# Kernel tuning notes

Hardware: AMD Instinct MI355X
Metric: run time of the kernel (lower is better)

Reference implementation:

```python
import jax, jax.numpy as jnp
import numpy as np

B, T, D, H = 32, 8192, 128, 128

def setup_inputs() -> dict:
    key = jax.random.key(0)
    k1, k2, k3, k4, k5 = jax.random.split(key, 5)
    return {
        "encoder_outputs": jax.random.normal(k1, (B, T, D), dtype=jnp.float32),
        "decoder_hidden": jax.random.normal(k2, (B, H), dtype=jnp.float32),
        "W1": jax.random.normal(k3, (D, D), dtype=jnp.float32) * 0.08,
        "W2": jax.random.normal(k4, (H, D), dtype=jnp.float32) * 0.08,
        "V": jax.random.normal(k5, (D, 1), dtype=jnp.float32) * 0.08,
    }

def reference(encoder_outputs, decoder_hidden, W1, W2, V):
    # score: [B, T, D] = tanh(enc @ W1 + (dec @ W2)[:, None, :])
    score = jnp.tanh(jnp.einsum('btd,de->bte', encoder_outputs, W1)
                     + jnp.einsum('bh,hd->bd', decoder_hidden, W2)[:, None, :])
    # logits: [B, T, 1]; softmax over time axis (axis=1)
    logits = jnp.einsum('btd,do->bto', score, V)
    attention_weights = jax.nn.softmax(logits, axis=1)
    # context: [B, D] weighted sum over T
    context_vector = jnp.sum(attention_weights * encoder_outputs, axis=1)
    return context_vector, attention_weights
```

## Files before the change

kernel.cpp:

```cpp
#include <hip/hip_runtime.h>

#define B_ 32
#define T_ 8192
#define D_ 128
#define MBLK 64
#define NCHUNK 128

typedef __attribute__((ext_vector_type(8))) _Float16 half8;
typedef __attribute__((ext_vector_type(4))) _Float16 half4;
typedef __attribute__((ext_vector_type(4))) float floatx4;

__device__ __forceinline__ float tanh_fast(float x) {
    float e = __expf(2.0f * x);
    return 1.0f - __fdividef(2.0f, e + 1.0f);
}

__global__ void frag_kernel(const float* __restrict__ W1, half8* __restrict__ W1frag) {
    int tg = blockIdx.x * 256 + threadIdx.x;
    int kk = tg >> 9, ni = (tg >> 6) & 7, lane = tg & 63;
    half8 h;
    #pragma unroll
    for (int j = 0; j < 8; ++j) {
        int k = kk * 32 + ((lane >> 4) * 8) + j;
        int n = ni * 16 + (lane & 15);
        h[j] = (_Float16)W1[k * 128 + n];
    }
    W1frag[tg] = h;
}

__global__ void bias_kernel(const float* __restrict__ dec, const float* __restrict__ W2,
                            float* __restrict__ bias) {
    int b = blockIdx.x, d = threadIdx.x;
    float acc = 0.f;
    for (int h = 0; h < 128; ++h)
        acc += dec[b * 128 + h] * W2[h * 128 + d];
    bias[b * 128 + d] = acc;
}

__global__ __launch_bounds__(256)
void main_kernel(const float* __restrict__ enc, const half8* __restrict__ W1frag,
                 const float* __restrict__ bias, const float* __restrict__ V,
                 float* __restrict__ out_w, float* __restrict__ m_part,
                 float* __restrict__ s_part, float* __restrict__ c_part)
{
    __shared__ __align__(16) _Float16 encl[MBLK * 128];
    __shared__ __align__(16) half8 bfr[2048];
    __shared__ float red[MBLK];
    __shared__ float c_red[8 * 128];

    const int tid = threadIdx.x;
    const int l = tid & 63;
    const int w = tid >> 6;
    const int bid = blockIdx.x;
    const int b = bid >> 7;
    const int chunk = bid & 127;
    const float* encp = enc + ((long)(b * T_) + chunk * MBLK) * D_;

    #pragma unroll
    for (int q = 0; q < 8; ++q)
        bfr[q * 256 + tid] = W1frag[q * 256 + tid];

    #pragma unroll
    for (int q = 0; q < 8; ++q) {
        int flat = (q * 256 + tid) * 4;
        int r = flat >> 7, c = flat & 127;
        float4 f = *(const float4*)(encp + flat);
        half4 h;
        h[0] = (_Float16)f.x; h[1] = (_Float16)f.y;
        h[2] = (_Float16)f.z; h[3] = (_Float16)f.w;
        int byte = r * 256 + ((c * 2) ^ ((r & 7) << 4));
        *(half4*)((char*)encl + byte) = h;
    }
    __syncthreads();

    floatx4 acc[8];
    #pragma unroll
    for (int ni = 0; ni < 8; ++ni) acc[ni] = (floatx4)0.0f;

    const int arow = w * 16 + (l & 15);
    const int asw = (arow & 7) << 4;
    const int abase = arow * 256;
    #pragma unroll
    for (int kk = 0; kk < 4; ++kk) {
        half8 a = *(const half8*)((char*)encl +
                   (abase + (((kk * 64) + ((l >> 4) * 16)) ^ asw)));
        #pragma unroll
        for (int ni = 0; ni < 8; ++ni)
            acc[ni] = __builtin_amdgcn_mfma_f32_16x16x32_f16(
                          a, bfr[(kk * 8 + ni) * 64 + l], acc[ni], 0, 0, 0);
    }

    float bs[8], vv[8];
    #pragma unroll
    for (int ni = 0; ni < 8; ++ni) {
        int n = ni * 16 + (l & 15);
        bs[ni] = bias[b * 128 + n];
        vv[ni] = V[n];
    }
    #pragma unroll
    for (int j2 = 0; j2 < 4; ++j2) {
        float p = 0.f;
        #pragma unroll
        for (int ni = 0; ni < 8; ++ni)
            p += tanh_fast(acc[ni][j2] + bs[ni]) * vv[ni];
        #pragma unroll
        for (int mk = 1; mk < 16; mk <<= 1)
            p += __shfl_xor(p, mk);
        if ((l & 15) == 0) {
            int r = w * 16 + (l >> 4) * 4 + j2;
            red[r] = p;
            out_w[(long)b * T_ + chunk * MBLK + r] = p;
        }
    }
    __syncthreads();

    if (tid < 64) {
        float lg = red[tid];
        float m = lg;
        #pragma unroll
        for (int mk = 1; mk < 64; mk <<= 1) m = fmaxf(m, __shfl_xor(m, mk));
        float ew = __expf(lg - m);
        float s = ew;
        #pragma unroll
        for (int mk = 1; mk < 64; mk <<= 1) s += __shfl_xor(s, mk);
        red[tid] = ew;
        if (tid == 0) { m_part[bid] = m; s_part[bid] = s; }
    }
    __syncthreads();

    {
        int c0 = (tid & 31) * 4, rg = tid >> 5;
        floatx4 cc = (floatx4)0.0f;
        #pragma unroll
        for (int rr = 0; rr < 8; ++rr) {
            int r = rg * 8 + rr;
            float wgt = red[r];
            half4 h = *(const half4*)((char*)encl +
                       (r * 256 + (((tid & 31) * 8) ^ ((r & 7) << 4))));
            #pragma unroll
            for (int i = 0; i < 4; ++i) cc[i] += wgt * (float)h[i];
        }
        *(floatx4*)(&c_red[rg * 128 + c0]) = cc;
    }
    __syncthreads();
    if (tid < 128) {
        float s = 0.f;
        #pragma unroll
        for (int g = 0; g < 8; ++g) s += c_red[g * 128 + tid];
        c_part[(long)bid * 128 + tid] = s;
    }
}

__global__ void reduce_kernel(const float* __restrict__ m_part, const float* __restrict__ s_part,
                              const float* __restrict__ c_part, float* __restrict__ ctx,
                              float* __restrict__ mg, float* __restrict__ sg)
{
    __shared__ float sm[128];
    __shared__ float sc[128];
    int b = blockIdx.x, i = threadIdx.x;
    float m = m_part[b * 128 + i];
    sm[i] = m;
    __syncthreads();
    for (int s = 64; s > 0; s >>= 1) {
        if (i < s) sm[i] = fmaxf(sm[i], sm[i + s]);
        __syncthreads();
    }
    float m_g = sm[0];
    __syncthreads();
    float e = __expf(m - m_g);
    sm[i] = s_part[b * 128 + i] * e;
    __syncthreads();
    for (int s = 64; s > 0; s >>= 1) {
        if (i < s) sm[i] += sm[i + s];
        __syncthreads();
    }
    float s_g = sm[0];
    __syncthreads();
    sc[i] = e / s_g;
    if (i == 0) { mg[b] = m_g; sg[b] = s_g; }
    __syncthreads();
    float acc = 0.f;
    for (int ch = 0; ch < 128; ++ch)
        acc += c_part[((long)b * 128 + ch) * 128 + i] * sc[ch];
    ctx[b * 128 + i] = acc;
}

__global__ void finalize_kernel(float* __restrict__ out_w, const float* __restrict__ mg,
                                const float* __restrict__ sg)
{
    int idx = blockIdx.x * 256 + threadIdx.x;
    int b = idx >> 13;
    float lg = out_w[idx];
    out_w[idx] = __expf(lg - mg[b]) / sg[b];
}

extern "C" void kernel_launch(void* const* d_in, const int* in_sizes, int n_in,
                              void* d_out, int out_size, void* d_ws, size_t ws_size,
                              hipStream_t stream)
{
    const float* enc = (const float*)d_in[0];
    const float* dec = (const float*)d_in[1];
    const float* W1  = (const float*)d_in[2];
    const float* W2  = (const float*)d_in[3];
    const float* V   = (const float*)d_in[4];

    float* ctx  = (float*)d_out;
    float* outw = ctx + B_ * D_;

    float* ws     = (float*)d_ws;
    float* bias   = ws;
    float* m_part = bias + 4096;
    float* s_part = m_part + 4096;
    float* mg     = s_part + 4096;
    float* sg     = mg + 32;
    float* c_part = sg + 32;
    half8* W1frag = (half8*)(c_part + (long)B_ * NCHUNK * 128);

    frag_kernel<<<8, 256, 0, stream>>>(W1, W1frag);
    bias_kernel<<<32, 128, 0, stream>>>(dec, W2, bias);
    main_kernel<<<B_ * NCHUNK, 256, 0, stream>>>(enc, W1frag, bias, V, outw, m_part, s_part, c_part);
    reduce_kernel<<<B_, 128, 0, stream>>>(m_part, s_part, c_part, ctx, mg, sg);
    finalize_kernel<<<(B_ * T_) / 256, 256, 0, stream>>>(outw, mg, sg);
}
```

Baseline: 59.12 us.

## Double rows per block, merge prep kernels, halve partial reductions

Each main-kernel block now processes 128 timesteps instead of 64, with each wave computing two 16-row MFMA tiles that share the same B-fragment loads. This halves the grid and the per-block W1 fragment staging overhead, and it halves the partial softmax/context outputs that the reduce kernel must combine. The frag and bias kernels are merged into one prep launch to save a launch. In exchange, LDS per block grows (the fp16 encoder tile doubles) and accumulator register pressure doubles, which may reduce occupancy.

```diff
diff --git a/kernel.cpp b/kernel.cpp
--- a/kernel.cpp
+++ b/kernel.cpp
@@ -3,8 +3,8 @@
 #define B_ 32
 #define T_ 8192
 #define D_ 128
-#define MBLK 64
-#define NCHUNK 128
+#define MBLK 128
+#define NCHUNK 64
 
 typedef __attribute__((ext_vector_type(8))) _Float16 half8;
 typedef __attribute__((ext_vector_type(4))) _Float16 half4;
@@ -15,26 +15,29 @@
     return 1.0f - __fdividef(2.0f, e + 1.0f);
 }
 
-__global__ void frag_kernel(const float* __restrict__ W1, half8* __restrict__ W1frag) {
-    int tg = blockIdx.x * 256 + threadIdx.x;
-    int kk = tg >> 9, ni = (tg >> 6) & 7, lane = tg & 63;
-    half8 h;
-    #pragma unroll
-    for (int j = 0; j < 8; ++j) {
-        int k = kk * 32 + ((lane >> 4) * 8) + j;
-        int n = ni * 16 + (lane & 15);
-        h[j] = (_Float16)W1[k * 128 + n];
-    }
-    W1frag[tg] = h;
-}
-
-__global__ void bias_kernel(const float* __restrict__ dec, const float* __restrict__ W2,
+__global__ void prep_kernel(const float* __restrict__ W1, half8* __restrict__ W1frag,
+                            const float* __restrict__ dec, const float* __restrict__ W2,
                             float* __restrict__ bias) {
-    int b = blockIdx.x, d = threadIdx.x;
-    float acc = 0.f;
-    for (int h = 0; h < 128; ++h)
-        acc += dec[b * 128 + h] * W2[h * 128 + d];
-    bias[b * 128 + d] = acc;
+    int bid = blockIdx.x, tid = threadIdx.x;
+    if (bid < 8) {
+        int tg = bid * 256 + tid;
+        int kk = tg >> 9, ni = (tg >> 6) & 7, lane = tg & 63;
+        half8 h;
+        #pragma unroll
+        for (int j = 0; j < 8; ++j) {
+            int k = kk * 32 + ((lane >> 4) * 8) + j;
+            int n = ni * 16 + (lane & 15);
+            h[j] = (_Float16)W1[k * 128 + n];
+        }
+        W1frag[tg] = h;
+    } else {
+        int b = (bid - 8) * 2 + (tid >> 7);
+        int d = tid & 127;
+        float acc = 0.f;
+        for (int h = 0; h < 128; ++h)
+            acc += dec[b * 128 + h] * W2[h * 128 + d];
+        bias[b * 128 + d] = acc;
+    }
 }
 
 __global__ __launch_bounds__(256)
@@ -52,8 +55,8 @@
     const int l = tid & 63;
     const int w = tid >> 6;
     const int bid = blockIdx.x;
-    const int b = bid >> 7;
-    const int chunk = bid & 127;
+    const int b = bid >> 6;
+    const int chunk = bid & 63;
     const float* encp = enc + ((long)(b * T_) + chunk * MBLK) * D_;
 
     #pragma unroll
@@ -61,7 +64,7 @@
         bfr[q * 256 + tid] = W1frag[q * 256 + tid];
 
     #pragma unroll
-    for (int q = 0; q < 8; ++q) {
+    for (int q = 0; q < 16; ++q) {
         int flat = (q * 256 + tid) * 4;
         int r = flat >> 7, c = flat & 127;
         float4 f = *(const float4*)(encp + flat);
@@ -73,21 +76,25 @@
     }
     __syncthreads();
 
-    floatx4 acc[8];
-    #pragma unroll
-    for (int ni = 0; ni < 8; ++ni) acc[ni] = (floatx4)0.0f;
-
-    const int arow = w * 16 + (l & 15);
+    floatx4 acc[2][8];
+    #pragma unroll
+    for (int si = 0; si < 2; ++si)
+        #pragma unroll
+        for (int ni = 0; ni < 8; ++ni) acc[si][ni] = (floatx4)0.0f;
+
+    const int arow = w * 32 + (l & 15);
     const int asw = (arow & 7) << 4;
-    const int abase = arow * 256;
     #pragma unroll
     for (int kk = 0; kk < 4; ++kk) {
-        half8 a = *(const half8*)((char*)encl +
-                   (abase + (((kk * 64) + ((l >> 4) * 16)) ^ asw)));
-        #pragma unroll
-        for (int ni = 0; ni < 8; ++ni)
-            acc[ni] = __builtin_amdgcn_mfma_f32_16x16x32_f16(
-                          a, bfr[(kk * 8 + ni) * 64 + l], acc[ni], 0, 0, 0);
+        int koff = (kk * 64 + ((l >> 4) * 16)) ^ asw;
+        half8 a0 = *(const half8*)((char*)encl + (arow * 256 + koff));
+        half8 a1 = *(const half8*)((char*)encl + ((arow + 16) * 256 + koff));
+        #pragma unroll
+        for (int ni = 0; ni < 8; ++ni) {
+            half8 bf = bfr[(kk * 8 + ni) * 64 + l];
+            acc[0][ni] = __builtin_amdgcn_mfma_f32_16x16x32_f16(a0, bf, acc[0][ni], 0, 0, 0);
+            acc[1][ni] = __builtin_amdgcn_mfma_f32_16x16x32_f16(a1, bf, acc[1][ni], 0, 0, 0);
+        }
     }
 
     float bs[8], vv[8];
@@ -98,32 +105,35 @@
         vv[ni] = V[n];
     }
     #pragma unroll
-    for (int j2 = 0; j2 < 4; ++j2) {
-        float p = 0.f;
-        #pragma unroll
-        for (int ni = 0; ni < 8; ++ni)
-            p += tanh_fast(acc[ni][j2] + bs[ni]) * vv[ni];
-        #pragma unroll
-        for (int mk = 1; mk < 16; mk <<= 1)
-            p += __shfl_xor(p, mk);
-        if ((l & 15) == 0) {
-            int r = w * 16 + (l >> 4) * 4 + j2;
-            red[r] = p;
-            out_w[(long)b * T_ + chunk * MBLK + r] = p;
+    for (int si = 0; si < 2; ++si) {
+        #pragma unroll
+        for (int j2 = 0; j2 < 4; ++j2) {
+            float p = 0.f;
+            #pragma unroll
+            for (int ni = 0; ni < 8; ++ni)
+                p += tanh_fast(acc[si][ni][j2] + bs[ni]) * vv[ni];
+            #pragma unroll
+            for (int mk = 1; mk < 16; mk <<= 1)
+                p += __shfl_xor(p, mk);
+            if ((l & 15) == 0) {
+                int r = w * 32 + si * 16 + (l >> 4) * 4 + j2;
+                red[r] = p;
+                out_w[(long)b * T_ + chunk * MBLK + r] = p;
+            }
         }
     }
     __syncthreads();
 
     if (tid < 64) {
-        float lg = red[tid];
-        float m = lg;
+        float l0 = red[tid], l1 = red[tid + 64];
+        float m = fmaxf(l0, l1);
         #pragma unroll
         for (int mk = 1; mk < 64; mk <<= 1) m = fmaxf(m, __shfl_xor(m, mk));
-        float ew = __expf(lg - m);
-        float s = ew;
+        float e0 = __expf(l0 - m), e1 = __expf(l1 - m);
+        float s = e0 + e1;
         #pragma unroll
         for (int mk = 1; mk < 64; mk <<= 1) s += __shfl_xor(s, mk);
-        red[tid] = ew;
+        red[tid] = e0; red[tid + 64] = e1;
         if (tid == 0) { m_part[bid] = m; s_part[bid] = s; }
     }
     __syncthreads();
@@ -132,8 +142,8 @@
         int c0 = (tid & 31) * 4, rg = tid >> 5;
         floatx4 cc = (floatx4)0.0f;
         #pragma unroll
-        for (int rr = 0; rr < 8; ++rr) {
-            int r = rg * 8 + rr;
+        for (int rr = 0; rr < 16; ++rr) {
+            int r = rg * 16 + rr;
             float wgt = red[r];
             half4 h = *(const half4*)((char*)encl +
                        (r * 256 + (((tid & 31) * 8) ^ ((r & 7) << 4))));
@@ -155,22 +165,22 @@
                               const float* __restrict__ c_part, float* __restrict__ ctx,
                               float* __restrict__ mg, float* __restrict__ sg)
 {
-    __shared__ float sm[128];
-    __shared__ float sc[128];
+    __shared__ float sm[64];
+    __shared__ float sc[64];
     int b = blockIdx.x, i = threadIdx.x;
-    float m = m_part[b * 128 + i];
+    float m = m_part[b * 64 + i];
     sm[i] = m;
     __syncthreads();
-    for (int s = 64; s > 0; s >>= 1) {
+    for (int s = 32; s > 0; s >>= 1) {
         if (i < s) sm[i] = fmaxf(sm[i], sm[i + s]);
         __syncthreads();
     }
     float m_g = sm[0];
     __syncthreads();
     float e = __expf(m - m_g);
-    sm[i] = s_part[b * 128 + i] * e;
-    __syncthreads();
-    for (int s = 64; s > 0; s >>= 1) {
+    sm[i] = s_part[b * 64 + i] * e;
+    __syncthreads();
+    for (int s = 32; s > 0; s >>= 1) {
         if (i < s) sm[i] += sm[i + s];
         __syncthreads();
     }
@@ -179,10 +189,14 @@
     sc[i] = e / s_g;
     if (i == 0) { mg[b] = m_g; sg[b] = s_g; }
     __syncthreads();
-    float acc = 0.f;
-    for (int ch = 0; ch < 128; ++ch)
-        acc += c_part[((long)b * 128 + ch) * 128 + i] * sc[ch];
-    ctx[b * 128 + i] = acc;
+    float acc0 = 0.f, acc1 = 0.f;
+    for (int ch = 0; ch < 64; ++ch) {
+        float w = sc[ch];
+        acc0 += c_part[((long)b * 64 + ch) * 128 + i] * w;
+        acc1 += c_part[((long)b * 64 + ch) * 128 + 64 + i] * w;
+    }
+    ctx[b * 128 + i] = acc0;
+    ctx[b * 128 + 64 + i] = acc1;
 }
 
 __global__ void finalize_kernel(float* __restrict__ out_w, const float* __restrict__ mg,
@@ -210,15 +224,14 @@
     float* ws     = (float*)d_ws;
     float* bias   = ws;
     float* m_part = bias + 4096;
-    float* s_part = m_part + 4096;
-    float* mg     = s_part + 4096;
+    float* s_part = m_part + 2048;
+    float* mg     = s_part + 2048;
     float* sg     = mg + 32;
     float* c_part = sg + 32;
     half8* W1frag = (half8*)(c_part + (long)B_ * NCHUNK * 128);
 
-    frag_kernel<<<8, 256, 0, stream>>>(W1, W1frag);
-    bias_kernel<<<32, 128, 0, stream>>>(dec, W2, bias);
+    prep_kernel<<<24, 256, 0, stream>>>(W1, W1frag, dec, W2, bias);
     main_kernel<<<B_ * NCHUNK, 256, 0, stream>>>(enc, W1frag, bias, V, outw, m_part, s_part, c_part);
-    reduce_kernel<<<B_, 128, 0, stream>>>(m_part, s_part, c_part, ctx, mg, sg);
+    reduce_kernel<<<B_, 64, 0, stream>>>(m_part, s_part, c_part, ctx, mg, sg);
     finalize_kernel<<<(B_ * T_) / 256, 256, 0, stream>>>(outw, mg, sg);
 }
```

New measurement: 58.45 us. About the same (-1.1%).
